# Kernel optimization log

Hardware: AMD Instinct MI355X
Metric: run time of the kernel (lower is better)

The kernel has to match this reference:

```python
import jax, jax.numpy as jnp
import numpy as np

NUM_EMBEDDINGS = 8192
EMBEDDING_DIM = 256
COMMITMENT_COST = 0.25


def setup_inputs() -> dict:
    key = jax.random.key(0)
    k1, k2 = jax.random.split(key)
    x = jax.random.normal(k1, (8, 4096, EMBEDDING_DIM), dtype=jnp.float32)
    # torch init: uniform(-1/K, 1/K)
    codebook = jax.random.uniform(
        k2, (NUM_EMBEDDINGS, EMBEDDING_DIM), dtype=jnp.float32,
        minval=-1.0 / NUM_EMBEDDINGS, maxval=1.0 / NUM_EMBEDDINGS)
    return {"x": x, "codebook": codebook}


def reference(x, codebook):
    D = codebook.shape[1]
    K = codebook.shape[0]
    flat_x = x.reshape(-1, D)                      # [N, D]
    distances = (jnp.sum(flat_x * flat_x, axis=1, keepdims=True)
                 + jnp.sum(codebook * codebook, axis=1)
                 - 2.0 * jnp.matmul(flat_x, codebook.T))
    encoding_indices = jnp.argmin(distances, axis=1)  # [N]
    # direct gather instead of one-hot matmul (same math)
    quantized = codebook[encoding_indices].reshape(x.shape)

    sg = jax.lax.stop_gradient
    e_latent_loss = jnp.mean((sg(quantized) - x) ** 2)
    q_latent_loss = jnp.mean((quantized - sg(x)) ** 2)
    loss = q_latent_loss + COMMITMENT_COST * e_latent_loss

    quantized_st = x + sg(quantized - x)

    # avg one-hot probs via counts
    counts = jnp.bincount(encoding_indices, length=K)
    avg_probs = counts.astype(x.dtype) / encoding_indices.shape[0]
    perplexity = jnp.exp(-jnp.sum(avg_probs * jnp.log(avg_probs + 1e-10)))
    return quantized_st, loss, perplexity
```

## Files before the change

kernel.cpp:

```cpp
#include <hip/hip_runtime.h>
#include <cfloat>
#include <math.h>

#define NUM_EMB 8192
#define DIM 256
#define NROWS 32768
#define NSPLIT 4
#define CHUNKS 16

typedef float f32x4 __attribute__((ext_vector_type(4)));
typedef int   i32x4 __attribute__((ext_vector_type(4)));
typedef int   i32x8 __attribute__((ext_vector_type(8)));

#define GL2LDS(g, l) __builtin_amdgcn_global_load_lds( \
    (const __attribute__((address_space(1))) void*)(g), \
    (__attribute__((address_space(3))) void*)(l), 16, 0, 0)

__global__ __launch_bounds__(256) void vq_prep(const float* __restrict__ x,
                                               unsigned char* __restrict__ xq,
                                               const float* __restrict__ cb,
                                               unsigned char* __restrict__ cbq,
                                               float* __restrict__ cbn,
                                               unsigned int* __restrict__ counts) {
    int b = blockIdx.x;
    if (b < 4096) {
        int i = b * 256 + threadIdx.x;
        float4 v0 = ((const float4*)x)[2 * i];
        float4 v1 = ((const float4*)x)[2 * i + 1];
        int p0 = __builtin_amdgcn_cvt_pk_fp8_f32(v0.x, v0.y, 0, false);
        p0     = __builtin_amdgcn_cvt_pk_fp8_f32(v0.z, v0.w, p0, true);
        int p1 = __builtin_amdgcn_cvt_pk_fp8_f32(v1.x, v1.y, 0, false);
        p1     = __builtin_amdgcn_cvt_pk_fp8_f32(v1.z, v1.w, p1, true);
        ((int2*)xq)[i] = make_int2(p0, p1);
    } else if (b < 6144) {
        int row  = (b - 4096) * 4 + (threadIdx.x >> 6);
        int lane = threadIdx.x & 63;
        float4 v = ((const float4*)(cb + (size_t)row * DIM))[lane];
        int p = __builtin_amdgcn_cvt_pk_fp8_f32(v.x * 8192.f, v.y * 8192.f, 0, false);
        p     = __builtin_amdgcn_cvt_pk_fp8_f32(v.z * 8192.f, v.w * 8192.f, p, true);
        ((int*)cbq)[row * 64 + lane] = p;
        float s = v.x * v.x + v.y * v.y + v.z * v.z + v.w * v.w;
        #pragma unroll
        for (int off = 32; off > 0; off >>= 1) s += __shfl_down(s, off, 64);
        if (lane == 0) cbn[row] = 8192.f * s + 512.f;
    } else {
        counts[(b - 6144) * 256 + threadIdx.x] = 0u;
    }
}

__global__ __launch_bounds__(256) void vq_argmin_mfma(
        const unsigned char* __restrict__ xq,
        const unsigned char* __restrict__ cbq,
        const float* __restrict__ cbn,
        unsigned long long* __restrict__ partial) {
    __shared__ __align__(16) unsigned char As[2][128 * 128];
    __shared__ __align__(16) unsigned char Bs[128 * 128];
    __shared__ unsigned long long redk[2][128];

    const int tid = threadIdx.x;
    const int lane = tid & 63;
    const int w = tid >> 6;
    const int wm = w >> 1, wn = w & 1;
    const int l15 = lane & 15, q = lane >> 4;
    const int ns = blockIdx.x & (NSPLIT - 1);
    const int by = blockIdx.x / NSPLIT;
    const int m0 = by * 128;
    const int nbase = ns * (NUM_EMB / NSPLIT);

    const int sub = lane >> 3;
    const int sl  = lane & 7;

    #pragma unroll
    for (int kc = 0; kc < 2; kc++)
        #pragma unroll
        for (int t = 0; t < 4; t++) {
            int seg = t * 4 + w;
            int row = seg * 8 + sub;
            int blk = sl ^ (row & 7);
            GL2LDS((const char*)xq + (size_t)(m0 + row) * 256 + kc * 128 + blk * 16,
                   (char*)As[kc] + seg * 1024);
        }

    unsigned int colb[4];
    #pragma unroll
    for (int j = 0; j < 4; j++) colb[j] = (unsigned)(wn * 64 + j * 16 + l15);

    unsigned int runk[4][4];
    #pragma unroll
    for (int i = 0; i < 4; i++)
        #pragma unroll
        for (int r = 0; r < 4; r++) runk[i][r] = 0xFFFFFFFFu;

    #pragma unroll 1
    for (int ch = 0; ch < CHUNKS; ch++) {
        const int n0c = nbase + ch * 128;
        const unsigned int chb = (unsigned)ch << 7;
        unsigned int cj[4];
        float bnj[4];
        #pragma unroll
        for (int j = 0; j < 4; j++) {
            cj[j] = chb | colb[j];
            bnj[j] = cbn[n0c + (int)colb[j]];
        }

        f32x4 acc[4][4];
        #pragma unroll
        for (int i = 0; i < 4; i++)
            #pragma unroll
            for (int j = 0; j < 4; j++) acc[i][j] = (f32x4)0.f;

        #pragma unroll
        for (int kc = 0; kc < 2; kc++) {
            __syncthreads();
            #pragma unroll
            for (int t = 0; t < 4; t++) {
                int seg = t * 4 + w;
                int row = seg * 8 + sub;
                int blk = sl ^ (row & 7);
                GL2LDS((const char*)cbq + (size_t)(n0c + row) * 256 + kc * 128 + blk * 16,
                       (char*)Bs + seg * 1024);
            }
            __syncthreads();

            i32x8 bfr[4];
            #pragma unroll
            for (int j = 0; j < 4; j++) {
                int row = wn * 64 + j * 16 + l15;
                int s0 = ((2 * q) ^ (row & 7)) * 16;
                int s1 = ((2 * q + 1) ^ (row & 7)) * 16;
                i32x4 lo = *(const i32x4*)(Bs + row * 128 + s0);
                i32x4 hi = *(const i32x4*)(Bs + row * 128 + s1);
                bfr[j] = __builtin_shufflevector(lo, hi, 0, 1, 2, 3, 4, 5, 6, 7);
            }
            #pragma unroll
            for (int i = 0; i < 4; i++) {
                int row = wm * 64 + i * 16 + l15;
                int s0 = ((2 * q) ^ (row & 7)) * 16;
                int s1 = ((2 * q + 1) ^ (row & 7)) * 16;
                i32x4 lo = *(const i32x4*)(As[kc] + row * 128 + s0);
                i32x4 hi = *(const i32x4*)(As[kc] + row * 128 + s1);
                i32x8 afr = __builtin_shufflevector(lo, hi, 0, 1, 2, 3, 4, 5, 6, 7);
                #pragma unroll
                for (int j = 0; j < 4; j++)
                    acc[i][j] = __builtin_amdgcn_mfma_scale_f32_16x16x128_f8f6f4(
                        afr, bfr[j], acc[i][j], 0, 0,
                        0, 127, 0, 127);
            }
        }

        #pragma unroll
        for (int i = 0; i < 4; i++) {
            #pragma unroll
            for (int r = 0; r < 4; r++) {
                unsigned int k0 = (__float_as_uint(fmaf(-2.f, acc[i][0][r], bnj[0])) & 0xFFFFF800u) | cj[0];
                unsigned int k1 = (__float_as_uint(fmaf(-2.f, acc[i][1][r], bnj[1])) & 0xFFFFF800u) | cj[1];
                unsigned int k2 = (__float_as_uint(fmaf(-2.f, acc[i][2][r], bnj[2])) & 0xFFFFF800u) | cj[2];
                unsigned int k3 = (__float_as_uint(fmaf(-2.f, acc[i][3][r], bnj[3])) & 0xFFFFF800u) | cj[3];
                runk[i][r] = min(runk[i][r], min(min(k0, k1), min(k2, k3)));
            }
        }
    }

    #pragma unroll
    for (int i = 0; i < 4; i++) {
        #pragma unroll
        for (int r = 0; r < 4; r++) {
            unsigned int rk = runk[i][r];
            unsigned int gcol = (unsigned)nbase + (rk & 0x7FFu);
            unsigned long long key =
                ((unsigned long long)(rk & 0xFFFFF800u) << 32) | gcol;
            #pragma unroll
            for (int off = 8; off >= 1; off >>= 1) {
                unsigned long long o = __shfl_xor(key, off, 16);
                if (o < key) key = o;
            }
            if (l15 == 0) redk[wn][wm * 64 + i * 16 + q * 4 + r] = key;
        }
    }
    __syncthreads();
    if (tid < 128) {
        unsigned long long k0 = redk[0][tid], k1 = redk[1][tid];
        partial[(size_t)ns * NROWS + m0 + tid] = k0 < k1 ? k0 : k1;
    }
}

__global__ __launch_bounds__(256) void vq_out(const float* __restrict__ x,
                                              const float* __restrict__ cb,
                                              const unsigned long long* __restrict__ partial,
                                              float* __restrict__ out,
                                              unsigned int* __restrict__ counts,
                                              double* __restrict__ loss_part) {
    __shared__ float wred[4];
    int wv   = threadIdx.x >> 6;
    int row  = blockIdx.x * 4 + wv;
    int lane = threadIdx.x & 63;
    unsigned long long k = 0xFFFFFFFFFFFFFFFFull;
    #pragma unroll
    for (int t = 0; t < NSPLIT; t++) {
        unsigned long long v = partial[(size_t)t * NROWS + row];
        if (v < k) k = v;
    }
    int id = (int)(unsigned int)(k & 0xffffffffu);
    float4 qv = ((const float4*)(cb + (size_t)id * DIM))[lane];
    float4 xv = ((const float4*)(x + (size_t)row * DIM))[lane];
    float dx = qv.x - xv.x, dy = qv.y - xv.y, dz = qv.z - xv.z, dw = qv.w - xv.w;
    float4 o;
    o.x = xv.x + dx; o.y = xv.y + dy; o.z = xv.z + dz; o.w = xv.w + dw;
    ((float4*)(out + (size_t)row * DIM))[lane] = o;
    float s = dx * dx + dy * dy + dz * dz + dw * dw;
    #pragma unroll
    for (int o2 = 32; o2 > 0; o2 >>= 1) s += __shfl_down(s, o2, 64);
    if (lane == 0) {
        wred[wv] = s;
        atomicAdd(&counts[id], 1u);
    }
    __syncthreads();
    if (threadIdx.x == 0) {
        loss_part[blockIdx.x] =
            (double)wred[0] + (double)wred[1] + (double)wred[2] + (double)wred[3];
    }
}

__global__ __launch_bounds__(256) void vq_fin(const unsigned int* __restrict__ counts,
                                              const double* __restrict__ loss_part,
                                              float* __restrict__ out_tail) {
    __shared__ double sh[256];
    __shared__ double sl[256];
    int tid = threadIdx.x;
    double h = 0.0;
    for (int k = tid; k < NUM_EMB; k += 256) {
        float p = (float)counts[k] / 32768.0f;
        h += (double)p * log((double)p + 1e-10);
    }
    double ls = 0.0;
    for (int b = tid; b < NROWS / 4; b += 256) ls += loss_part[b];
    sh[tid] = h;
    sl[tid] = ls;
    __syncthreads();
    for (int o = 128; o > 0; o >>= 1) {
        if (tid < o) { sh[tid] += sh[tid + o]; sl[tid] += sl[tid + o]; }
        __syncthreads();
    }
    if (tid == 0) {
        double mean = sl[0] / (double)((size_t)NROWS * DIM);
        out_tail[0] = (float)(1.25 * mean);
        out_tail[1] = (float)exp(-sh[0]);
    }
}

extern "C" void kernel_launch(void* const* d_in, const int* in_sizes, int n_in,
                              void* d_out, int out_size, void* d_ws, size_t ws_size,
                              hipStream_t stream) {
    const float* x  = (const float*)d_in[0];
    const float* cb = (const float*)d_in[1];
    char* ws = (char*)d_ws;
    unsigned int* counts   = (unsigned int*)(ws + 256);
    float* cbn             = (float*)(ws + 33024);
    unsigned char* xq      = (unsigned char*)(ws + 65792);
    unsigned char* cbq     = (unsigned char*)(ws + 65792 + 8388608);
    unsigned long long* pp = (unsigned long long*)(ws + 65792 + 8388608 + 2097152);
    double* loss_part      = (double*)(ws + 65792 + 8388608 + 2097152 + 16777216);
    float* out = (float*)d_out;

    vq_prep       <<<6176, 256, 0, stream>>>(x, xq, cb, cbq, cbn, counts);
    vq_argmin_mfma<<<256 * NSPLIT, 256, 0, stream>>>(xq, cbq, cbn, pp);
    vq_out        <<<8192, 256, 0, stream>>>(x, cb, pp, out, counts, loss_part);
    vq_fin        <<<1, 256, 0, stream>>>(counts, loss_part, out + (size_t)NROWS * DIM);
}
```

Baseline: 212.6 us.

## Shrink argmin M-tile to 64 rows, keep A in registers, load full-K B tile

The argmin kernel now handles 64 rows per block instead of 128, doubling the grid. The x fragments are loaded once directly into registers rather than staged through LDS. The codebook tile is loaded for the full K=256 in one stage per chunk, which halves the barriers per chunk. Launch bounds request 4 blocks per SM to raise occupancy. In exchange, each codebook tile is reused by half as many rows, so codebook traffic from L2 doubles and MFMA work per B fragment load is lower.

Result: no change. 211.6 us (-0.5%).

```diff
diff --git a/kernel.cpp b/kernel.cpp
--- a/kernel.cpp
+++ b/kernel.cpp
@@ -48,14 +48,13 @@
     }
 }
 
-__global__ __launch_bounds__(256) void vq_argmin_mfma(
+__global__ __launch_bounds__(256, 4) void vq_argmin_mfma(
         const unsigned char* __restrict__ xq,
         const unsigned char* __restrict__ cbq,
         const float* __restrict__ cbn,
         unsigned long long* __restrict__ partial) {
-    __shared__ __align__(16) unsigned char As[2][128 * 128];
-    __shared__ __align__(16) unsigned char Bs[128 * 128];
-    __shared__ unsigned long long redk[2][128];
+    __shared__ __align__(16) unsigned char Bs[128 * 256];
+    __shared__ unsigned long long redk[2][64];
 
     const int tid = threadIdx.x;
     const int lane = tid & 63;
@@ -64,32 +63,33 @@
     const int l15 = lane & 15, q = lane >> 4;
     const int ns = blockIdx.x & (NSPLIT - 1);
     const int by = blockIdx.x / NSPLIT;
-    const int m0 = by * 128;
+    const int m0 = by * 64;
     const int nbase = ns * (NUM_EMB / NSPLIT);
 
-    const int sub = lane >> 3;
-    const int sl  = lane & 7;
-
+    i32x8 afr[2][2];
     #pragma unroll
     for (int kc = 0; kc < 2; kc++)
         #pragma unroll
-        for (int t = 0; t < 4; t++) {
-            int seg = t * 4 + w;
-            int row = seg * 8 + sub;
-            int blk = sl ^ (row & 7);
-            GL2LDS((const char*)xq + (size_t)(m0 + row) * 256 + kc * 128 + blk * 16,
-                   (char*)As[kc] + seg * 1024);
+        for (int i = 0; i < 2; i++) {
+            const unsigned char* p =
+                xq + (size_t)(m0 + wm * 32 + i * 16 + l15) * 256 + kc * 128 + q * 32;
+            i32x4 lo = *(const i32x4*)p;
+            i32x4 hi = *(const i32x4*)(p + 16);
+            afr[kc][i] = __builtin_shufflevector(lo, hi, 0, 1, 2, 3, 4, 5, 6, 7);
         }
 
     unsigned int colb[4];
     #pragma unroll
     for (int j = 0; j < 4; j++) colb[j] = (unsigned)(wn * 64 + j * 16 + l15);
 
-    unsigned int runk[4][4];
-    #pragma unroll
-    for (int i = 0; i < 4; i++)
+    unsigned int runk[2][4];
+    #pragma unroll
+    for (int i = 0; i < 2; i++)
         #pragma unroll
         for (int r = 0; r < 4; r++) runk[i][r] = 0xFFFFFFFFu;
+
+    const int sr = lane >> 4;
+    const int sv = lane & 15;
 
     #pragma unroll 1
     for (int ch = 0; ch < CHUNKS; ch++) {
@@ -103,53 +103,43 @@
             bnj[j] = cbn[n0c + (int)colb[j]];
         }
 
-        f32x4 acc[4][4];
-        #pragma unroll
-        for (int i = 0; i < 4; i++)
+        f32x4 acc[2][4];
+        #pragma unroll
+        for (int i = 0; i < 2; i++)
             #pragma unroll
             for (int j = 0; j < 4; j++) acc[i][j] = (f32x4)0.f;
 
+        __syncthreads();
+        #pragma unroll
+        for (int t = 0; t < 8; t++) {
+            int s = t * 4 + w;
+            int row = s * 4 + sr;
+            int kcs = sv >> 3, blk = sv & 7;
+            GL2LDS(cbq + (size_t)(n0c + row) * 256 + kcs * 128 + ((blk ^ (row & 7)) * 16),
+                   (char*)Bs + s * 1024);
+        }
+        __syncthreads();
+
         #pragma unroll
         for (int kc = 0; kc < 2; kc++) {
-            __syncthreads();
-            #pragma unroll
-            for (int t = 0; t < 4; t++) {
-                int seg = t * 4 + w;
-                int row = seg * 8 + sub;
-                int blk = sl ^ (row & 7);
-                GL2LDS((const char*)cbq + (size_t)(n0c + row) * 256 + kc * 128 + blk * 16,
-                       (char*)Bs + seg * 1024);
-            }
-            __syncthreads();
-
-            i32x8 bfr[4];
             #pragma unroll
             for (int j = 0; j < 4; j++) {
                 int row = wn * 64 + j * 16 + l15;
+                int base = row * 256 + kc * 128;
                 int s0 = ((2 * q) ^ (row & 7)) * 16;
                 int s1 = ((2 * q + 1) ^ (row & 7)) * 16;
-                i32x4 lo = *(const i32x4*)(Bs + row * 128 + s0);
-                i32x4 hi = *(const i32x4*)(Bs + row * 128 + s1);
-                bfr[j] = __builtin_shufflevector(lo, hi, 0, 1, 2, 3, 4, 5, 6, 7);
+                i32x4 lo = *(const i32x4*)(Bs + base + s0);
+                i32x4 hi = *(const i32x4*)(Bs + base + s1);
+                i32x8 bfr = __builtin_shufflevector(lo, hi, 0, 1, 2, 3, 4, 5, 6, 7);
+                acc[0][j] = __builtin_amdgcn_mfma_scale_f32_16x16x128_f8f6f4(
+                    afr[kc][0], bfr, acc[0][j], 0, 0, 0, 127, 0, 127);
+                acc[1][j] = __builtin_amdgcn_mfma_scale_f32_16x16x128_f8f6f4(
+                    afr[kc][1], bfr, acc[1][j], 0, 0, 0, 127, 0, 127);
             }
-            #pragma unroll
-            for (int i = 0; i < 4; i++) {
-                int row = wm * 64 + i * 16 + l15;
-                int s0 = ((2 * q) ^ (row & 7)) * 16;
-                int s1 = ((2 * q + 1) ^ (row & 7)) * 16;
-                i32x4 lo = *(const i32x4*)(As[kc] + row * 128 + s0);
-                i32x4 hi = *(const i32x4*)(As[kc] + row * 128 + s1);
-                i32x8 afr = __builtin_shufflevector(lo, hi, 0, 1, 2, 3, 4, 5, 6, 7);
-                #pragma unroll
-                for (int j = 0; j < 4; j++)
-                    acc[i][j] = __builtin_amdgcn_mfma_scale_f32_16x16x128_f8f6f4(
-                        afr, bfr[j], acc[i][j], 0, 0,
-                        0, 127, 0, 127);
-            }
-        }
-
-        #pragma unroll
-        for (int i = 0; i < 4; i++) {
+        }
+
+        #pragma unroll
+        for (int i = 0; i < 2; i++) {
             #pragma unroll
             for (int r = 0; r < 4; r++) {
                 unsigned int k0 = (__float_as_uint(fmaf(-2.f, acc[i][0][r], bnj[0])) & 0xFFFFF800u) | cj[0];
@@ -162,7 +152,7 @@
     }
 
     #pragma unroll
-    for (int i = 0; i < 4; i++) {
+    for (int i = 0; i < 2; i++) {
         #pragma unroll
         for (int r = 0; r < 4; r++) {
             unsigned int rk = runk[i][r];
@@ -174,11 +164,11 @@
                 unsigned long long o = __shfl_xor(key, off, 16);
                 if (o < key) key = o;
             }
-            if (l15 == 0) redk[wn][wm * 64 + i * 16 + q * 4 + r] = key;
+            if (l15 == 0) redk[wn][wm * 32 + i * 16 + q * 4 + r] = key;
         }
     }
     __syncthreads();
-    if (tid < 128) {
+    if (tid < 64) {
         unsigned long long k0 = redk[0][tid], k1 = redk[1][tid];
         partial[(size_t)ns * NROWS + m0 + tid] = k0 < k1 ? k0 : k1;
     }
@@ -263,7 +253,7 @@
     float* out = (float*)d_out;
 
     vq_prep       <<<6176, 256, 0, stream>>>(x, xq, cb, cbq, cbn, counts);
-    vq_argmin_mfma<<<256 * NSPLIT, 256, 0, stream>>>(xq, cbq, cbn, pp);
+    vq_argmin_mfma<<<512 * NSPLIT, 256, 0, stream>>>(xq, cbq, cbn, pp);
     vq_out        <<<8192, 256, 0, stream>>>(x, cb, pp, out, counts, loss_part);
     vq_fin        <<<1, 256, 0, stream>>>(counts, loss_part, out + (size_t)NROWS * DIM);
 }
```
